# Optimization experiments

Hardware: AMD Instinct MI355X
Metric: run time of the kernel (lower is better)

The kernel has to match this reference:

```python
import jax, jax.numpy as jnp
import numpy as np


def _scinol_new_p(p0, S2, G, eta, M, cond):
    # SCINOL effective-parameter computation (done under no_grad in torch)
    denom = jnp.sqrt(S2 + M * M)
    theta = jnp.clip(G / denom, -1.0, 1.0)
    upd = jnp.where(cond, theta / (2.0 * denom) * eta, 0.0)
    return p0 + jax.lax.stop_gradient(upd)


def _conv(x, w, b):
    y = jax.lax.conv_general_dilated(x, w, window_strides=(1, 1), padding='VALID',
                                     dimension_numbers=('NCHW', 'OIHW', 'NCHW'))
    return y + b[None, :, None, None]


def _maxpool2(x):
    return jax.lax.reduce_window(x, -jnp.inf, jax.lax.max, (1, 1, 2, 2), (1, 1, 2, 2), 'VALID')


def _scinol_conv(x, w0, wS2, wG, weta, wM, b0, bS2, bG, beta):
    # M-update: per-input-channel mean (over batch) of max-abs over H,W
    stat = jax.lax.stop_gradient(jnp.mean(jnp.max(jnp.abs(x), axis=(2, 3)), axis=0))  # (C_in,)
    M = jnp.maximum(stat, wM)  # (C_in,)
    w = _scinol_new_p(w0, wS2, wG, weta, M[None, :, None, None], wG != 0)
    b = _scinol_new_p(b0, bS2, bG, beta, jnp.float32(1.0), bG != 0)
    return _conv(x, w, b)


def _scinol_linear(x, w0, wS2, wG, weta, wM, b0, bS2, bG, beta):
    stat = jax.lax.stop_gradient(jnp.mean(jnp.abs(x), axis=0))  # (in_features,)
    M = jnp.maximum(wM, stat)  # broadcast -> (out, in)
    w = _scinol_new_p(w0, wS2, wG, weta, M, wS2 != 0)
    b = _scinol_new_p(b0, bS2, bG, beta, jnp.float32(1.0), bS2 != 0)
    return x @ w.T + b


def setup_inputs() -> dict:
    key = jax.random.key(0)
    ks = iter(jax.random.split(key, 40))
    f32 = jnp.float32
    d = {}
    d['x'] = jax.random.normal(next(ks), (2048, 1, 28, 28), dtype=f32)
    for pre, wshape, cin in [('c1', (64, 1, 5, 5), 1), ('c2', (64, 64, 5, 5), 64)]:
        d[pre + '_w0'] = jax.random.normal(next(ks), wshape, dtype=f32) * 0.1
        d[pre + '_wS2'] = jax.random.uniform(next(ks), wshape, dtype=f32)
        d[pre + '_wG'] = jax.random.normal(next(ks), wshape, dtype=f32)
        d[pre + '_weta'] = jax.random.uniform(next(ks), wshape, dtype=f32)
        d[pre + '_wM'] = jax.random.uniform(next(ks), (cin,), dtype=f32)
        d[pre + '_b0'] = jax.random.normal(next(ks), (64,), dtype=f32) * 0.1
        d[pre + '_bS2'] = jax.random.uniform(next(ks), (64,), dtype=f32)
        d[pre + '_bG'] = jax.random.normal(next(ks), (64,), dtype=f32)
        d[pre + '_beta'] = jax.random.uniform(next(ks), (64,), dtype=f32)
    d['l_w0'] = jax.random.normal(next(ks), (10, 1024), dtype=f32) * 0.03
    d['l_wS2'] = jax.random.uniform(next(ks), (10, 1024), dtype=f32)
    d['l_wG'] = jax.random.normal(next(ks), (10, 1024), dtype=f32)
    d['l_weta'] = jax.random.uniform(next(ks), (10, 1024), dtype=f32)
    d['l_wM'] = jax.random.uniform(next(ks), (10, 1024), dtype=f32)
    d['l_b0'] = jax.random.normal(next(ks), (10,), dtype=f32) * 0.03
    d['l_bS2'] = jax.random.uniform(next(ks), (10,), dtype=f32)
    d['l_bG'] = jax.random.normal(next(ks), (10,), dtype=f32)
    d['l_beta'] = jax.random.uniform(next(ks), (10,), dtype=f32)
    return d


def reference(x,
              c1_w0, c1_wS2, c1_wG, c1_weta, c1_wM, c1_b0, c1_bS2, c1_bG, c1_beta,
              c2_w0, c2_wS2, c2_wG, c2_weta, c2_wM, c2_b0, c2_bS2, c2_bG, c2_beta,
              l_w0, l_wS2, l_wG, l_weta, l_wM, l_b0, l_bS2, l_bG, l_beta):
    h = _scinol_conv(x, c1_w0, c1_wS2, c1_wG, c1_weta, c1_wM, c1_b0, c1_bS2, c1_bG, c1_beta)
    h = _maxpool2(jax.nn.relu(h))                      # (N,64,12,12)
    h = _scinol_conv(h, c2_w0, c2_wS2, c2_wG, c2_weta, c2_wM, c2_b0, c2_bS2, c2_bG, c2_beta)
    h = _maxpool2(jax.nn.relu(h))                      # (N,64,4,4)
    h = h.reshape(h.shape[0], -1)                      # (N,1024)
    return _scinol_linear(h, l_w0, l_wS2, l_wG, l_weta, l_wM, l_b0, l_bS2, l_bG, l_beta)
```

## Files before the change

kernel.cpp:

```cpp
#include <hip/hip_runtime.h>
#include <hip/hip_bf16.h>

typedef float v4f __attribute__((ext_vector_type(4)));
typedef short v8s __attribute__((ext_vector_type(8)));

#define WS_STAT2   0
#define WS_STATL   64
#define WS_B1      1088
#define WS_B2      1152
#define WS_WL      1216
#define WS_BL      11456
#define WS_IMAX    11520
#define WS_W1F_B   54272
#define WS_WP2_B   62464
#define WS_P1_B    267264
#define WS_P2_B    38016000
#define WS_C1MAX_F 9504000
#define WS_LPART_F 66816

__global__ void k_stat1(const float* __restrict__ x, float* ws) {
    int tid = threadIdx.x;
    int wv = tid >> 6, lane = tid & 63;
    int n = blockIdx.x * 4 + wv;
    const float* p = x + n * 784;
    float m = 0.f;
    for (int i = lane; i < 784; i += 64) m = fmaxf(m, fabsf(p[i]));
#pragma unroll
    for (int off = 32; off; off >>= 1) m = fmaxf(m, __shfl_xor(m, off, 64));
    if (lane == 0) ws[WS_IMAX + n] = m;
}

__global__ void k_prepw1(const float* __restrict__ w0, const float* __restrict__ S2,
                         const float* __restrict__ G, const float* __restrict__ eta,
                         const float* __restrict__ wM,
                         const float* __restrict__ b0, const float* __restrict__ bS2,
                         const float* __restrict__ bG, const float* __restrict__ beta,
                         float* ws) {
    __shared__ float red[256];
    int tid = threadIdx.x;
    float p = 0.f;
    for (int i = tid; i < 2048; i += 256) p += ws[WS_IMAX + i];
    red[tid] = p;
    __syncthreads();
    for (int s = 128; s > 0; s >>= 1) {
        if (tid < s) red[tid] += red[tid + s];
        __syncthreads();
    }
    float M = fmaxf(red[0] * (1.f / 2048.f), wM[0]);

    int i = blockIdx.x * 256 + tid;
    if (i < 4096) {
        int j = i & 7, m16 = (i >> 3) & 15, q = (i >> 7) & 3, ot = i >> 9;
        int tap = q * 8 + j, oc = m16 * 4 + ot;
        float v = 0.f;
        if (tap < 25) {
            int s = oc * 25 + tap;
            float g = G[s];
            float den = sqrtf(S2[s] + M * M);
            float inv = 1.f / den;
            float th = fminf(fmaxf(g * inv, -1.f), 1.f);
            v = w0[s] + ((g != 0.f) ? th * 0.5f * inv * eta[s] : 0.f);
        }
        ((__hip_bfloat16*)((char*)ws + WS_W1F_B))[i] = __float2bfloat16(v);
    } else if (i < 4160) {
        int c = i - 4096;
        float g = bG[c];
        float den = sqrtf(bS2[c] + 1.f);
        float inv = 1.f / den;
        float th = fminf(fmaxf(g * inv, -1.f), 1.f);
        ws[WS_B1 + c] = b0[c] + ((g != 0.f) ? th * 0.5f * inv * beta[c] : 0.f);
    }
}

__global__ void __launch_bounds__(256)
k_conv1(const float* __restrict__ x, float* ws, __hip_bfloat16* __restrict__ pool1) {
    __shared__ __align__(16) float sX[1024];
    __shared__ int sMax[64];
    int n = blockIdx.x, tid = threadIdx.x;
    int wv = tid >> 6, lane = tid & 63;
    int m16 = lane & 15, quad = lane >> 4;

    {
        const float4* src = (const float4*)(x + (size_t)n * 784);
        float4 v = {0.f, 0.f, 0.f, 0.f};
        if (tid < 196) v = src[tid];
        ((float4*)sX)[tid] = v;
    }
    if (tid < 64) sMax[tid] = 0;

    const ushort* wfrag = (const ushort*)((const char*)ws + WS_W1F_B);
    v8s bfr[4];
#pragma unroll
    for (int ot = 0; ot < 4; ++ot)
        bfr[ot] = *(const v8s*)(wfrag + ((ot * 4 + quad) * 16 + m16) * 8);
    float4 bias = *(const float4*)(ws + WS_B1 + m16 * 4);

    int dj[8];
#pragma unroll
    for (int j = 0; j < 8; ++j) {
        int tap = quad * 8 + j;
        int u = (tap * 13) >> 6;
        dj[j] = tap + 23 * u;
    }

    int W0 = wv * 36 + (m16 >> 2);
    int wy = (W0 * 171) >> 11;
    int wx = W0 - wy * 12;
    int coff = 28 * ((m16 >> 1) & 1) + (m16 & 1);

    __syncthreads();

    float vmax[4] = {0.f, 0.f, 0.f, 0.f};
    ushort* op = (ushort*)(pool1 + (size_t)n * 9216);

    float g[8];
    {
        int base = 56 * wy + 2 * wx + coff;
#pragma unroll
        for (int j = 0; j < 8; ++j) g[j] = sX[base + dj[j]];
    }
    for (int mt = 0; mt < 9; ++mt) {
        union { v8s v; ushort us[8]; } ua;
#pragma unroll
        for (int j = 0; j < 8; ++j)
            ua.us[j] = __bfloat16_as_ushort(__float2bfloat16(g[j]));

        wx += 4;
        if (wx >= 12) { wx -= 12; ++wy; }
        if (mt < 8) {
            int nb = 56 * wy + 2 * wx + coff;
#pragma unroll
            for (int j = 0; j < 8; ++j) g[j] = sX[nb + dj[j]];
        }

        v4f z = {0.f, 0.f, 0.f, 0.f};
        v4f acc[4];
#pragma unroll
        for (int ot = 0; ot < 4; ++ot)
            acc[ot] = __builtin_amdgcn_mfma_f32_16x16x32_bf16(ua.v, bfr[ot], z, 0, 0, 0);

        int Wd = (wv * 9 + mt) * 4 + quad;
        ushort4 pk;
#pragma unroll
        for (int ot = 0; ot < 4; ++ot) {
            v4f a = acc[ot];
            float m = fmaxf(fmaxf(a[0], a[1]), fmaxf(a[2], a[3]));
            float pv = fmaxf(m + bias[ot], 0.f);
            vmax[ot] = fmaxf(vmax[ot], pv);
            ((ushort*)&pk)[ot] = __bfloat16_as_ushort(__float2bfloat16(pv));
        }
        *(ushort4*)(op + Wd * 64 + m16 * 4) = pk;
    }

#pragma unroll
    for (int ot = 0; ot < 4; ++ot) {
        float m = vmax[ot];
        m = fmaxf(m, __shfl_xor(m, 16, 64));
        m = fmaxf(m, __shfl_xor(m, 32, 64));
        if (lane < 16) atomicMax(&sMax[lane * 4 + ot], __float_as_int(m));
    }
    __syncthreads();
    if (tid < 64) ws[WS_C1MAX_F + n * 64 + tid] = __int_as_float(sMax[tid]);
}

__global__ void k_stat2red(float* ws) {
    __shared__ float red[256];
    int c = blockIdx.x, t = threadIdx.x;
    float s = 0.f;
    for (int n = t; n < 2048; n += 256) s += ws[WS_C1MAX_F + n * 64 + c];
    red[t] = s;
    __syncthreads();
    for (int k = 128; k > 0; k >>= 1) {
        if (t < k) red[t] += red[t + k];
        __syncthreads();
    }
    if (t == 0) ws[WS_STAT2 + c] = red[0] * (1.f / 2048.f);
}

__global__ void k_prepw2(const float* __restrict__ w0, const float* __restrict__ S2,
                         const float* __restrict__ G, const float* __restrict__ eta,
                         const float* __restrict__ wM,
                         const float* __restrict__ b0, const float* __restrict__ bS2,
                         const float* __restrict__ bG, const float* __restrict__ beta,
                         float* ws, __hip_bfloat16* __restrict__ wp2) {
    int i = blockIdx.x * 256 + threadIdx.x;
    int j = i & 7, m16 = (i >> 3) & 15, quad = (i >> 7) & 3;
    int ot = (i >> 9) & 3, kc = (i >> 11) & 1, uv = i >> 12;
    int oc = ot * 16 + m16, ic = kc * 32 + quad * 8 + j;
    int s = oc * 1600 + ic * 25 + uv;
    float M = fmaxf(ws[WS_STAT2 + ic], wM[ic]);
    float g = G[s];
    float den = sqrtf(S2[s] + M * M);
    float inv = 1.f / den;
    float th = fminf(fmaxf(g * inv, -1.f), 1.f);
    float v = w0[s] + ((g != 0.f) ? th * 0.5f * inv * eta[s] : 0.f);
    wp2[i] = __float2bfloat16(v);
    if (blockIdx.x == 0 && threadIdx.x < 64) {
        int c = threadIdx.x;
        float gb = bG[c];
        float den2 = sqrtf(bS2[c] + 1.f);
        float inv2 = 1.f / den2;
        float th2 = fminf(fmaxf(gb * inv2, -1.f), 1.f);
        ws[WS_B2 + c] = b0[c] + ((gb != 0.f) ? th2 * 0.5f * inv2 * beta[c] : 0.f);
    }
}

__global__ void __launch_bounds__(256, 2)
k_conv2(const ushort* __restrict__ pool1, const ushort* __restrict__ wp2,
        const float* __restrict__ ws, float* __restrict__ pool2) {
    __shared__ __align__(16) ushort sImg[4 * 9216];
    __shared__ __align__(16) ushort sB[4096];
    int tid = threadIdx.x;
    int wv = tid >> 6, lane = tid & 63;
    int n0 = blockIdx.x * 4;

    {
        const uint4* src = (const uint4*)(pool1 + (size_t)n0 * 9216);
        uint4* dst = (uint4*)sImg;
#pragma unroll
        for (int img = 0; img < 4; ++img) {
            int b = img * 1152;
#pragma unroll
            for (int i = 0; i < 4; ++i) {
                int c = tid + i * 256;
                int r = c >> 3, col = c & 7;
                dst[b + r * 8 + (col ^ (r & 7))] = src[b + c];
            }
            if (tid < 128) {
                int c = 1024 + tid;
                int r = c >> 3, col = c & 7;
                dst[b + r * 8 + (col ^ (r & 7))] = src[b + c];
            }
        }
    }

    int m16 = lane & 15, quad = lane >> 4;
    int x0 = m16 & 7;
    int yb = m16 >> 3;
    int rbase = yb * 12 + x0;

    v4f acc[4][4];
#pragma unroll
    for (int i = 0; i < 4; ++i)
#pragma unroll
        for (int j = 0; j < 4; ++j) acc[i][j] = (v4f){0.f, 0.f, 0.f, 0.f};

    const uint4* bsrc = (const uint4*)wp2;
    uint4 br0 = bsrc[tid], br1 = bsrc[256 + tid];

    __syncthreads();
    ((uint4*)sB)[tid] = br0;
    ((uint4*)sB)[256 + tid] = br1;
    __syncthreads();

    const ushort* simg = sImg + wv * 9216;

    for (int uv = 0; uv < 25; ++uv) {
        uint4 nr0, nr1;
        if (uv < 24) {
            const uint4* nb = bsrc + (uv + 1) * 512;
            nr0 = nb[tid];
            nr1 = nb[256 + tid];
        }
        int u = (uv * 13) >> 6;
        int v = uv - u * 5;
        int r0_ = rbase + u * 12 + v;
#pragma unroll
        for (int kc = 0; kc < 2; ++kc) {
            v8s pA[4], pB[4];
#pragma unroll
            for (int pt = 0; pt < 4; ++pt) {
                int row = r0_ + pt * 24;
                int rs = row & 7;
                pA[pt] = *(const v8s*)(simg + row * 64 + (((kc * 4 + quad) ^ rs) << 3));
            }
#pragma unroll
            for (int ot = 0; ot < 4; ++ot)
                pB[ot] = *(const v8s*)(sB + (kc * 4 + ot) * 512 + lane * 8);
#pragma unroll
            for (int pt = 0; pt < 4; ++pt)
#pragma unroll
                for (int ot = 0; ot < 4; ++ot)
                    acc[pt][ot] = __builtin_amdgcn_mfma_f32_16x16x32_bf16(
                        pA[pt], pB[ot], acc[pt][ot], 0, 0, 0);
        }
        if (uv < 24) {
            __syncthreads();
            ((uint4*)sB)[tid] = nr0;
            ((uint4*)sB)[256 + tid] = nr1;
            __syncthreads();
        }
    }

    int n = n0 + wv;
    float bv[4];
#pragma unroll
    for (int ot = 0; ot < 4; ++ot) bv[ot] = ws[WS_B2 + ot * 16 + m16];
    float* outp = pool2 + (size_t)n * 1024;
#pragma unroll
    for (int pt = 0; pt < 4; ++pt)
#pragma unroll
        for (int ot = 0; ot < 4; ++ot) {
            v4f a = acc[pt][ot];
            float m01 = fmaxf(a[0], a[1]);
            float m23 = fmaxf(a[2], a[3]);
            m01 = fmaxf(m01, __shfl_xor(m01, 32, 64));
            m23 = fmaxf(m23, __shfl_xor(m23, 32, 64));
            if (lane < 32) {
                int oc = ot * 16 + m16;
                int f = oc * 16 + pt * 4 + (quad & 1) * 2;
                outp[f] = fmaxf(m01 + bv[ot], 0.f);
                outp[f + 1] = fmaxf(m23 + bv[ot], 0.f);
            }
        }
}

__global__ void k_statl(const float* __restrict__ pool2, float* ws) {
    int b = blockIdx.x, tid = threadIdx.x;
    float4 s = {0.f, 0.f, 0.f, 0.f};
    for (int im = 0; im < 32; ++im) {
        float4 v = ((const float4*)(pool2 + (size_t)(b * 32 + im) * 1024))[tid];
        s.x += v.x; s.y += v.y; s.z += v.z; s.w += v.w;
    }
    ((float4*)(ws + WS_LPART_F + b * 1024))[tid] = s;
}

__global__ void k_prepwl(const float* __restrict__ w0, const float* __restrict__ S2,
                         const float* __restrict__ G, const float* __restrict__ eta,
                         const float* __restrict__ wM,
                         const float* __restrict__ b0, const float* __restrict__ bS2,
                         const float* __restrict__ bG, const float* __restrict__ beta,
                         float* ws) {
    int i = blockIdx.x * 256 + threadIdx.x;
    if (i < 10240) {
        int f = i & 1023;
        float s = 0.f;
#pragma unroll
        for (int b = 0; b < 64; ++b) s += ws[WS_LPART_F + b * 1024 + f];
        float stat = s * (1.f / 2048.f);
        float M = fmaxf(wM[i], stat);
        float s2 = S2[i];
        float den = sqrtf(s2 + M * M);
        float inv = 1.f / den;
        float th = fminf(fmaxf(G[i] * inv, -1.f), 1.f);
        ws[WS_WL + i] = w0[i] + ((s2 != 0.f) ? th * 0.5f * inv * eta[i] : 0.f);
    } else if (i < 10250) {
        int c = i - 10240;
        float s2 = bS2[c];
        float den = sqrtf(s2 + 1.f);
        float inv = 1.f / den;
        float th = fminf(fmaxf(bG[c] * inv, -1.f), 1.f);
        ws[WS_BL + c] = b0[c] + ((s2 != 0.f) ? th * 0.5f * inv * beta[c] : 0.f);
    }
}

__global__ void k_linear(const float* __restrict__ pool2, const float* __restrict__ ws,
                         float* __restrict__ out) {
    int tid = threadIdx.x;
    int wv = tid >> 6, lane = tid & 63;
    int n = blockIdx.x * 4 + wv;
    const float* hp = pool2 + (size_t)n * 1024;
    float h[16];
#pragma unroll
    for (int j = 0; j < 16; ++j) h[j] = hp[j * 64 + lane];
    for (int oc = 0; oc < 10; ++oc) {
        const float* wp = ws + WS_WL + oc * 1024;
        float d = 0.f;
#pragma unroll
        for (int j = 0; j < 16; ++j) d = fmaf(h[j], wp[j * 64 + lane], d);
#pragma unroll
        for (int off = 32; off; off >>= 1) d += __shfl_xor(d, off, 64);
        if (lane == 0) out[n * 10 + oc] = d + ws[WS_BL + oc];
    }
}

extern "C" void kernel_launch(void* const* d_in, const int* in_sizes, int n_in,
                              void* d_out, int out_size, void* d_ws, size_t ws_size,
                              hipStream_t stream) {
    const float* x = (const float*)d_in[0];
    float* ws = (float*)d_ws;
    __hip_bfloat16* wp2 = (__hip_bfloat16*)((char*)d_ws + WS_WP2_B);
    __hip_bfloat16* p1 = (__hip_bfloat16*)((char*)d_ws + WS_P1_B);
    float* p2 = (float*)((char*)d_ws + WS_P2_B);
    float* out = (float*)d_out;

    k_stat1<<<512, 256, 0, stream>>>(x, ws);
    k_prepw1<<<17, 256, 0, stream>>>(
        (const float*)d_in[1], (const float*)d_in[2], (const float*)d_in[3],
        (const float*)d_in[4], (const float*)d_in[5], (const float*)d_in[6],
        (const float*)d_in[7], (const float*)d_in[8], (const float*)d_in[9], ws);
    k_conv1<<<2048, 256, 0, stream>>>(x, ws, p1);
    k_stat2red<<<64, 256, 0, stream>>>(ws);
    k_prepw2<<<400, 256, 0, stream>>>(
        (const float*)d_in[10], (const float*)d_in[11], (const float*)d_in[12],
        (const float*)d_in[13], (const float*)d_in[14], (const float*)d_in[15],
        (const float*)d_in[16], (const float*)d_in[17], (const float*)d_in[18], ws, wp2);
    k_conv2<<<512, 256, 0, stream>>>((const ushort*)p1, (const ushort*)wp2, ws, p2);
    k_statl<<<64, 256, 0, stream>>>(p2, ws);
    k_prepwl<<<41, 256, 0, stream>>>(
        (const float*)d_in[19], (const float*)d_in[20], (const float*)d_in[21],
        (const float*)d_in[22], (const float*)d_in[23], (const float*)d_in[24],
        (const float*)d_in[25], (const float*)d_in[26], (const float*)d_in[27], ws);
    k_linear<<<512, 256, 0, stream>>>(p2, ws, out);
}
```

Baseline: 198.4 us.

## Fuse stat reductions into convs via atomics and stream conv2 input from global

Removes the k_stat2red and k_statl kernels. conv1 now atomically accumulates the per-channel mean max into the workspace, and conv2 atomically accumulates the linear-layer feature sums, with zeroing moved into earlier kernels. conv1 stores its input tile in LDS as bf16. conv2 no longer stages the four images in LDS: it loads A fragments straight from global and double-buffers the weight tile so there is one barrier per tap instead of two. This cuts launches and LDS footprint, so occupancy can rise, but it adds heavy global atomic contention (2048×1024 atomics into 1024 addresses), makes float summation order nondeterministic, and conv2 A loads become uncoalesced global reads.

After: 720.6 us. 263% more time.

```diff
diff --git a/kernel.cpp b/kernel.cpp
--- a/kernel.cpp
+++ b/kernel.cpp
@@ -15,13 +15,12 @@
 #define WS_WP2_B   62464
 #define WS_P1_B    267264
 #define WS_P2_B    38016000
-#define WS_C1MAX_F 9504000
-#define WS_LPART_F 66816
 
 __global__ void k_stat1(const float* __restrict__ x, float* ws) {
     int tid = threadIdx.x;
     int wv = tid >> 6, lane = tid & 63;
     int n = blockIdx.x * 4 + wv;
+    if (blockIdx.x == 0 && tid < 64) ws[WS_STAT2 + tid] = 0.f;
     const float* p = x + n * 784;
     float m = 0.f;
     for (int i = lane; i < 784; i += 64) m = fmaxf(m, fabsf(p[i]));
@@ -74,7 +73,7 @@
 
 __global__ void __launch_bounds__(256)
 k_conv1(const float* __restrict__ x, float* ws, __hip_bfloat16* __restrict__ pool1) {
-    __shared__ __align__(16) float sX[1024];
+    __shared__ __align__(16) ushort sXh[1024];
     __shared__ int sMax[64];
     int n = blockIdx.x, tid = threadIdx.x;
     int wv = tid >> 6, lane = tid & 63;
@@ -84,7 +83,12 @@
         const float4* src = (const float4*)(x + (size_t)n * 784);
         float4 v = {0.f, 0.f, 0.f, 0.f};
         if (tid < 196) v = src[tid];
-        ((float4*)sX)[tid] = v;
+        ushort4 h;
+        h.x = __bfloat16_as_ushort(__float2bfloat16(v.x));
+        h.y = __bfloat16_as_ushort(__float2bfloat16(v.y));
+        h.z = __bfloat16_as_ushort(__float2bfloat16(v.z));
+        h.w = __bfloat16_as_ushort(__float2bfloat16(v.w));
+        ((ushort4*)sXh)[tid] = h;
     }
     if (tid < 64) sMax[tid] = 0;
 
@@ -113,24 +117,23 @@
     float vmax[4] = {0.f, 0.f, 0.f, 0.f};
     ushort* op = (ushort*)(pool1 + (size_t)n * 9216);
 
-    float g[8];
+    ushort g[8];
     {
         int base = 56 * wy + 2 * wx + coff;
 #pragma unroll
-        for (int j = 0; j < 8; ++j) g[j] = sX[base + dj[j]];
+        for (int j = 0; j < 8; ++j) g[j] = sXh[base + dj[j]];
     }
     for (int mt = 0; mt < 9; ++mt) {
         union { v8s v; ushort us[8]; } ua;
 #pragma unroll
-        for (int j = 0; j < 8; ++j)
-            ua.us[j] = __bfloat16_as_ushort(__float2bfloat16(g[j]));
+        for (int j = 0; j < 8; ++j) ua.us[j] = g[j];
 
         wx += 4;
         if (wx >= 12) { wx -= 12; ++wy; }
         if (mt < 8) {
             int nb = 56 * wy + 2 * wx + coff;
 #pragma unroll
-            for (int j = 0; j < 8; ++j) g[j] = sX[nb + dj[j]];
+            for (int j = 0; j < 8; ++j) g[j] = sXh[nb + dj[j]];
         }
 
         v4f z = {0.f, 0.f, 0.f, 0.f};
@@ -160,21 +163,8 @@
         if (lane < 16) atomicMax(&sMax[lane * 4 + ot], __float_as_int(m));
     }
     __syncthreads();
-    if (tid < 64) ws[WS_C1MAX_F + n * 64 + tid] = __int_as_float(sMax[tid]);
-}
-
-__global__ void k_stat2red(float* ws) {
-    __shared__ float red[256];
-    int c = blockIdx.x, t = threadIdx.x;
-    float s = 0.f;
-    for (int n = t; n < 2048; n += 256) s += ws[WS_C1MAX_F + n * 64 + c];
-    red[t] = s;
-    __syncthreads();
-    for (int k = 128; k > 0; k >>= 1) {
-        if (t < k) red[t] += red[t + k];
-        __syncthreads();
-    }
-    if (t == 0) ws[WS_STAT2 + c] = red[0] * (1.f / 2048.f);
+    if (tid < 64)
+        atomicAdd(&ws[WS_STAT2 + tid], __int_as_float(sMax[tid]) * (1.f / 2048.f));
 }
 
 __global__ void k_prepw2(const float* __restrict__ w0, const float* __restrict__ S2,
@@ -203,41 +193,30 @@
         float th2 = fminf(fmaxf(gb * inv2, -1.f), 1.f);
         ws[WS_B2 + c] = b0[c] + ((gb != 0.f) ? th2 * 0.5f * inv2 * beta[c] : 0.f);
     }
-}
-
-__global__ void __launch_bounds__(256, 2)
+    if (blockIdx.x == 1) {
+#pragma unroll
+        for (int k = 0; k < 4; ++k) ws[WS_STATL + threadIdx.x + k * 256] = 0.f;
+    }
+}
+
+__global__ void __launch_bounds__(256)
 k_conv2(const ushort* __restrict__ pool1, const ushort* __restrict__ wp2,
-        const float* __restrict__ ws, float* __restrict__ pool2) {
-    __shared__ __align__(16) ushort sImg[4 * 9216];
-    __shared__ __align__(16) ushort sB[4096];
+        float* __restrict__ ws, float* __restrict__ pool2) {
+    __shared__ __align__(16) ushort sB[2][4096];
     int tid = threadIdx.x;
     int wv = tid >> 6, lane = tid & 63;
-    int n0 = blockIdx.x * 4;
-
+    int n = blockIdx.x * 4 + wv;
+    int m16 = lane & 15, quad = lane >> 4;
+    int q8 = quad * 8;
+    int x0 = m16 & 7, yb = m16 >> 3;
+    int rbase = yb * 12 + x0;
+
+    const uint4* bsrc = (const uint4*)wp2;
     {
-        const uint4* src = (const uint4*)(pool1 + (size_t)n0 * 9216);
-        uint4* dst = (uint4*)sImg;
-#pragma unroll
-        for (int img = 0; img < 4; ++img) {
-            int b = img * 1152;
-#pragma unroll
-            for (int i = 0; i < 4; ++i) {
-                int c = tid + i * 256;
-                int r = c >> 3, col = c & 7;
-                dst[b + r * 8 + (col ^ (r & 7))] = src[b + c];
-            }
-            if (tid < 128) {
-                int c = 1024 + tid;
-                int r = c >> 3, col = c & 7;
-                dst[b + r * 8 + (col ^ (r & 7))] = src[b + c];
-            }
-        }
-    }
-
-    int m16 = lane & 15, quad = lane >> 4;
-    int x0 = m16 & 7;
-    int yb = m16 >> 3;
-    int rbase = yb * 12 + x0;
+        uint4 b0 = bsrc[tid], b1 = bsrc[256 + tid];
+        ((uint4*)sB[0])[tid] = b0;
+        ((uint4*)sB[0])[256 + tid] = b1;
+    }
 
     v4f acc[4][4];
 #pragma unroll
@@ -245,16 +224,11 @@
 #pragma unroll
         for (int j = 0; j < 4; ++j) acc[i][j] = (v4f){0.f, 0.f, 0.f, 0.f};
 
-    const uint4* bsrc = (const uint4*)wp2;
-    uint4 br0 = bsrc[tid], br1 = bsrc[256 + tid];
+    const ushort* img = pool1 + (size_t)n * 9216;
 
     __syncthreads();
-    ((uint4*)sB)[tid] = br0;
-    ((uint4*)sB)[256 + tid] = br1;
-    __syncthreads();
-
-    const ushort* simg = sImg + wv * 9216;
-
+
+    int cur = 0;
     for (int uv = 0; uv < 25; ++uv) {
         uint4 nr0, nr1;
         if (uv < 24) {
@@ -264,35 +238,43 @@
         }
         int u = (uv * 13) >> 6;
         int v = uv - u * 5;
-        int r0_ = rbase + u * 12 + v;
-#pragma unroll
-        for (int kc = 0; kc < 2; ++kc) {
-            v8s pA[4], pB[4];
-#pragma unroll
-            for (int pt = 0; pt < 4; ++pt) {
-                int row = r0_ + pt * 24;
-                int rs = row & 7;
-                pA[pt] = *(const v8s*)(simg + row * 64 + (((kc * 4 + quad) ^ rs) << 3));
-            }
+        int r0 = rbase + u * 12 + v;
+
+        v8s a0[4], a1[4];
+#pragma unroll
+        for (int pt = 0; pt < 4; ++pt) {
+            const ushort* rp = img + (r0 + pt * 24) * 64 + q8;
+            a0[pt] = *(const v8s*)(rp);
+            a1[pt] = *(const v8s*)(rp + 32);
+        }
+        const ushort* sbc = sB[cur] + lane * 8;
+        v8s pB0[4], pB1[4];
+#pragma unroll
+        for (int ot = 0; ot < 4; ++ot) {
+            pB0[ot] = *(const v8s*)(sbc + ot * 512);
+            pB1[ot] = *(const v8s*)(sbc + (4 + ot) * 512);
+        }
+#pragma unroll
+        for (int pt = 0; pt < 4; ++pt)
 #pragma unroll
             for (int ot = 0; ot < 4; ++ot)
-                pB[ot] = *(const v8s*)(sB + (kc * 4 + ot) * 512 + lane * 8);
-#pragma unroll
-            for (int pt = 0; pt < 4; ++pt)
-#pragma unroll
-                for (int ot = 0; ot < 4; ++ot)
-                    acc[pt][ot] = __builtin_amdgcn_mfma_f32_16x16x32_bf16(
-                        pA[pt], pB[ot], acc[pt][ot], 0, 0, 0);
-        }
+                acc[pt][ot] = __builtin_amdgcn_mfma_f32_16x16x32_bf16(
+                    a0[pt], pB0[ot], acc[pt][ot], 0, 0, 0);
+#pragma unroll
+        for (int pt = 0; pt < 4; ++pt)
+#pragma unroll
+            for (int ot = 0; ot < 4; ++ot)
+                acc[pt][ot] = __builtin_amdgcn_mfma_f32_16x16x32_bf16(
+                    a1[pt], pB1[ot], acc[pt][ot], 0, 0, 0);
+
         if (uv < 24) {
-            __syncthreads();
-            ((uint4*)sB)[tid] = nr0;
-            ((uint4*)sB)[256 + tid] = nr1;
-            __syncthreads();
-        }
-    }
-
-    int n = n0 + wv;
+            ((uint4*)sB[cur ^ 1])[tid] = nr0;
+            ((uint4*)sB[cur ^ 1])[256 + tid] = nr1;
+        }
+        __syncthreads();
+        cur ^= 1;
+    }
+
     float bv[4];
 #pragma unroll
     for (int ot = 0; ot < 4; ++ot) bv[ot] = ws[WS_B2 + ot * 16 + m16];
@@ -309,20 +291,14 @@
             if (lane < 32) {
                 int oc = ot * 16 + m16;
                 int f = oc * 16 + pt * 4 + (quad & 1) * 2;
-                outp[f] = fmaxf(m01 + bv[ot], 0.f);
-                outp[f + 1] = fmaxf(m23 + bv[ot], 0.f);
+                float v0 = fmaxf(m01 + bv[ot], 0.f);
+                float v1 = fmaxf(m23 + bv[ot], 0.f);
+                outp[f] = v0;
+                outp[f + 1] = v1;
+                atomicAdd(&ws[WS_STATL + f], v0);
+                atomicAdd(&ws[WS_STATL + f + 1], v1);
             }
         }
-}
-
-__global__ void k_statl(const float* __restrict__ pool2, float* ws) {
-    int b = blockIdx.x, tid = threadIdx.x;
-    float4 s = {0.f, 0.f, 0.f, 0.f};
-    for (int im = 0; im < 32; ++im) {
-        float4 v = ((const float4*)(pool2 + (size_t)(b * 32 + im) * 1024))[tid];
-        s.x += v.x; s.y += v.y; s.z += v.z; s.w += v.w;
-    }
-    ((float4*)(ws + WS_LPART_F + b * 1024))[tid] = s;
 }
 
 __global__ void k_prepwl(const float* __restrict__ w0, const float* __restrict__ S2,
@@ -334,10 +310,7 @@
     int i = blockIdx.x * 256 + threadIdx.x;
     if (i < 10240) {
         int f = i & 1023;
-        float s = 0.f;
-#pragma unroll
-        for (int b = 0; b < 64; ++b) s += ws[WS_LPART_F + b * 1024 + f];
-        float stat = s * (1.f / 2048.f);
+        float stat = ws[WS_STATL + f] * (1.f / 2048.f);
         float M = fmaxf(wM[i], stat);
         float s2 = S2[i];
         float den = sqrtf(s2 + M * M);
@@ -390,13 +363,11 @@
         (const float*)d_in[4], (const float*)d_in[5], (const float*)d_in[6],
         (const float*)d_in[7], (const float*)d_in[8], (const float*)d_in[9], ws);
     k_conv1<<<2048, 256, 0, stream>>>(x, ws, p1);
-    k_stat2red<<<64, 256, 0, stream>>>(ws);
     k_prepw2<<<400, 256, 0, stream>>>(
         (const float*)d_in[10], (const float*)d_in[11], (const float*)d_in[12],
         (const float*)d_in[13], (const float*)d_in[14], (const float*)d_in[15],
         (const float*)d_in[16], (const float*)d_in[17], (const float*)d_in[18], ws, wp2);
     k_conv2<<<512, 256, 0, stream>>>((const ushort*)p1, (const ushort*)wp2, ws, p2);
-    k_statl<<<64, 256, 0, stream>>>(p2, ws);
     k_prepwl<<<41, 256, 0, stream>>>(
         (const float*)d_in[19], (const float*)d_in[20], (const float*)d_in[21],
         (const float*)d_in[22], (const float*)d_in[23], (const float*)d_in[24],
```
